# Optimization experiments

Hardware: AMD Instinct MI355X
Metric: run time of the kernel (lower is better)

The kernel has to match this reference:

```python
import jax, jax.numpy as jnp
import numpy as np

N_QUBITS = 20
EVO_SUPPORT = (2, 5)
CHAIN_QUBIT = 0


def _apply_operator(state, op, support):
    """Apply batched operator op (2^k, 2^k, B) to state (2,)*n + (B,) on `support` qubits.

    Faithful to pyqtorch's apply_operator: reshape op to (2,)*2k + (B,) and contract
    the support axes, keeping the batch axis aligned.
    """
    n = state.ndim - 1
    k = len(support)
    B = state.shape[-1]
    op = op.reshape((2,) * (2 * k) + (B,))
    letters = 'abcdefghijklmnopqrstuvwxyz'
    s_l = list(letters[:n])          # state qubit axes
    b = letters[n]                   # batch axis
    out_l = list(letters[n + 1:n + 1 + k])
    in_l = [s_l[q] for q in support]
    op_str = ''.join(out_l) + ''.join(in_l) + b
    st_str = ''.join(s_l) + b
    res = list(s_l)
    for q, o in zip(support, out_l):
        res[q] = o
    return jnp.einsum(f"{op_str},{st_str}->{''.join(res) + b}", op, state)


def setup_inputs() -> dict:
    key = jax.random.key(0)
    ks = jax.random.split(key, 6)
    B = 16
    dim = 2 ** N_QUBITS
    return {
        'state_re': jax.random.normal(ks[0], (dim, B), jnp.float32),
        'state_im': jax.random.normal(ks[1], (dim, B), jnp.float32),
        'hmat_re': jax.random.normal(ks[2], (4, 4, B), jnp.float32),
        'hmat_im': jax.random.normal(ks[3], (4, 4, B), jnp.float32),
        'theta': jax.random.uniform(ks[4], (8, B), jnp.float32),
        'tvals': jax.random.uniform(ks[5], (B,), jnp.float32),
    }


def reference(state_re, state_im, hmat_re, hmat_im, theta, tvals):
    n = N_QUBITS
    B = state_re.shape[-1]
    state = (state_re + 1j * state_im).astype(jnp.complex64).reshape((2,) * n + (B,))

    # --- PyQComposedBlock: chain of single-qubit RX gates composed via reduce(bmm, reversed) ---
    half = 0.5 * theta                      # (N_ops, B)
    c = jnp.cos(half).astype(jnp.complex64)
    s = jnp.sin(half).astype(jnp.complex64)
    # U_k: [[c, -i s], [-i s, c]] per op, batch-first layout (N_ops, B, 2, 2)
    U = jnp.stack([jnp.stack([c, -1j * s], axis=-1),
                   jnp.stack([-1j * s, c], axis=-1)], axis=-2)
    acc = U[-1]
    for i in range(U.shape[0] - 2, -1, -1):  # reduce(bmm, reversed(ops)): U_{N-1} @ ... @ U_0
        acc = acc @ U[i]
    state = _apply_operator(state, jnp.moveaxis(acc, 0, -1), (CHAIN_QUBIT,))

    # --- PyQHamiltonianEvolution: U = exp(-i t H) on a 2-qubit support ---
    A = (hmat_re + 1j * hmat_im).astype(jnp.complex64)       # (4, 4, B)
    H = 0.5 * (A + jnp.conj(jnp.swapaxes(A, 0, 1)))          # Hermitian generator
    Hb = jnp.moveaxis(H, -1, 0)                              # (B, 4, 4)
    evals, V = jnp.linalg.eigh(Hb)                           # H Hermitian -> exact matrix exp
    phase = jnp.exp(-1j * tvals[:, None] * evals)            # (B, 4)
    Ue = jnp.einsum('bij,bj,bkj->bik', V, phase.astype(jnp.complex64), jnp.conj(V))
    state = _apply_operator(state, jnp.moveaxis(Ue, 0, -1), EVO_SUPPORT)

    # --- Observable: total magnetization sum_q Z_q (AddPyQOperation of diagonal Z ops) ---
    w = jnp.zeros((2,) * n, jnp.float32)
    z = jnp.array([1.0, -1.0], jnp.float32)
    for q in range(n):
        w = w + z.reshape((1,) * q + (2,) + (1,) * (n - 1 - q))
    opsi = state * w[..., None]
    # expectation Re<psi|O|psi> per batch element
    return jnp.real(jnp.sum(jnp.conj(state) * opsi, axis=tuple(range(n))))
```

## Files before the change

### kernel.cpp

```cpp
#include <hip/hip_runtime.h>
#include <math.h>

constexpr int NQ     = 20;
constexpr int DIM    = 1 << NQ;
constexpr int B      = 16;
constexpr int GROUPS = 1 << 17;
constexpr int NBLK   = 1024;
constexpr int NTHR   = 512;


__global__ void prep_kernel(const float* __restrict__ hre, const float* __restrict__ him,
                            const float* __restrict__ theta, const float* __restrict__ tv,
                            float* __restrict__ ws) {
  int b = threadIdx.x;
  if (b >= B) return;

  double th = 0.0;
  for (int k = 0; k < 8; k++) th += (double)theta[k * B + b];
  th *= 0.5;
  ws[b]     = (float)cos(th);
  ws[B + b] = (float)sin(th);

  double t = (double)tv[b];
  double Mre[4][4], Mim[4][4];
  for (int i = 0; i < 4; i++)
    for (int j = 0; j < 4; j++) {
      double are = hre[(i*4+j)*B + b], aim = him[(i*4+j)*B + b];
      double cre = hre[(j*4+i)*B + b], cim = him[(j*4+i)*B + b];
      double Hre = 0.5*(are + cre), Him = 0.5*(aim - cim);
      Mre[i][j] = t * Him;
      Mim[i][j] = -t * Hre;
    }

  double ninf = 0.0;
  for (int i = 0; i < 4; i++) {
    double r = 0.0;
    for (int j = 0; j < 4; j++) r += fabs(Mre[i][j]) + fabs(Mim[i][j]);
    ninf = fmax(ninf, r);
  }
  int sc = 0;
  while (ninf > 0.25 && sc < 40) { ninf *= 0.5; sc++; }
  double scale = ldexp(1.0, -sc);
  for (int i = 0; i < 4; i++)
    for (int j = 0; j < 4; j++) { Mre[i][j] *= scale; Mim[i][j] *= scale; }

  double Tre[4][4], Tim[4][4];
  for (int i = 0; i < 4; i++)
    for (int j = 0; j < 4; j++) { Tre[i][j] = (i==j) ? 1.0 : 0.0; Tim[i][j] = 0.0; }
  for (int k = 13; k >= 1; k--) {
    double Pre[4][4], Pim[4][4];
    double inv = 1.0 / (double)k;
    for (int i = 0; i < 4; i++)
      for (int j = 0; j < 4; j++) {
        double rr = 0.0, ii = 0.0;
        for (int m = 0; m < 4; m++) {
          rr += Mre[i][m]*Tre[m][j] - Mim[i][m]*Tim[m][j];
          ii += Mre[i][m]*Tim[m][j] + Mim[i][m]*Tre[m][j];
        }
        Pre[i][j] = rr*inv + ((i==j) ? 1.0 : 0.0);
        Pim[i][j] = ii*inv;
      }
    for (int i = 0; i < 4; i++)
      for (int j = 0; j < 4; j++) { Tre[i][j] = Pre[i][j]; Tim[i][j] = Pim[i][j]; }
  }
  for (int q = 0; q < sc; q++) {
    double Pre[4][4], Pim[4][4];
    for (int i = 0; i < 4; i++)
      for (int j = 0; j < 4; j++) {
        double rr = 0.0, ii = 0.0;
        for (int m = 0; m < 4; m++) {
          rr += Tre[i][m]*Tre[m][j] - Tim[i][m]*Tim[m][j];
          ii += Tre[i][m]*Tim[m][j] + Tim[i][m]*Tre[m][j];
        }
        Pre[i][j] = rr; Pim[i][j] = ii;
      }
    for (int i = 0; i < 4; i++)
      for (int j = 0; j < 4; j++) { Tre[i][j] = Pre[i][j]; Tim[i][j] = Pim[i][j]; }
  }

  float* ue = ws + 2*B + b*32;
  for (int i = 0; i < 4; i++)
    for (int j = 0; j < 4; j++) {
      ue[(i*4+j)*2]     = (float)Tre[i][j];
      ue[(i*4+j)*2 + 1] = (float)Tim[i][j];
    }
}

#define RXPAIR(j, f) { \
  float xr = R[j].f, xi = I[j].f, yr = R[(j)+4].f, yi = I[(j)+4].f; \
  R[j].f     = fmaf(c4.f, xr,  s4.f * yi); \
  I[j].f     = fmaf(c4.f, xi, -s4.f * yr); \
  R[(j)+4].f = fmaf(s4.f, xi,  c4.f * yr); \
  I[(j)+4].f = fmaf(c4.f, yi, -s4.f * xr); \
}

#define UE_BI(f, bi, accv) \
  float accv = 0.f; \
  { \
    const float* ub = &u_lds[(b0 + (bi)) * 36]; \
    _Pragma("unroll") \
    for (int k = 0; k < 4; k++) { \
      float4 u0 = *(const float4*)(ub + 8*k);        \
      float4 u1 = *(const float4*)(ub + 8*k + 4);    \
      float rr0 = fmaf(u0.x, R[0].f, -u0.y * I[0].f); \
      rr0 = fmaf(u0.z, R[1].f, rr0); rr0 = fmaf(-u0.w, I[1].f, rr0); \
      rr0 = fmaf(u1.x, R[2].f, rr0); rr0 = fmaf(-u1.y, I[2].f, rr0); \
      rr0 = fmaf(u1.z, R[3].f, rr0); rr0 = fmaf(-u1.w, I[3].f, rr0); \
      float ii0 = fmaf(u0.x, I[0].f, u0.y * R[0].f); \
      ii0 = fmaf(u0.z, I[1].f, ii0); ii0 = fmaf(u0.w, R[1].f, ii0); \
      ii0 = fmaf(u1.x, I[2].f, ii0); ii0 = fmaf(u1.y, R[2].f, ii0); \
      ii0 = fmaf(u1.z, I[3].f, ii0); ii0 = fmaf(u1.w, R[3].f, ii0); \
      float rr1 = fmaf(u0.x, R[4].f, -u0.y * I[4].f); \
      rr1 = fmaf(u0.z, R[5].f, rr1); rr1 = fmaf(-u0.w, I[5].f, rr1); \
      rr1 = fmaf(u1.x, R[6].f, rr1); rr1 = fmaf(-u1.y, I[6].f, rr1); \
      rr1 = fmaf(u1.z, R[7].f, rr1); rr1 = fmaf(-u1.w, I[7].f, rr1); \
      float ii1 = fmaf(u0.x, I[4].f, u0.y * R[4].f); \
      ii1 = fmaf(u0.z, I[5].f, ii1); ii1 = fmaf(u0.w, R[5].f, ii1); \
      ii1 = fmaf(u1.x, I[6].f, ii1); ii1 = fmaf(u1.y, R[6].f, ii1); \
      ii1 = fmaf(u1.z, I[7].f, ii1); ii1 = fmaf(u1.w, R[7].f, ii1); \
      int sb = (k & 1) + (k >> 1); \
      float w0 = wb + (float)(3 - 2*sb);             \
      accv = fmaf(fmaf(rr0, rr0, ii0*ii0), w0,       accv); \
      accv = fmaf(fmaf(rr1, rr1, ii1*ii1), w0 - 2.f, accv); \
    } \
  }

__global__ __launch_bounds__(NTHR) void fused_kernel(
    const float* __restrict__ sre, const float* __restrict__ sim,
    const float* __restrict__ ws, float* __restrict__ partial) {
  __shared__ float u_lds[16 * 36];
  __shared__ float cs_lds[32];
  __shared__ float red[16];

  int t = threadIdx.x;
  {
    int b = t >> 5, e = t & 31;
    u_lds[b * 36 + e] = ws[2 * B + b * 32 + e];
  }
  if (t < 32) cs_lds[t] = ws[t];
  if (t < 16) red[t] = 0.f;
  __syncthreads();

  int tid = blockIdx.x * NTHR + t;
  int g   = tid >> 2;
  int b0  = (tid & 3) << 2;
  int base = (g & 0x3FFF) | ((g & 0xC000) << 1) | ((g & 0x10000) << 2);
  const float* pr = sre + base * B + b0;
  const float* pi = sim + base * B + b0;

  float4 R[8], I[8];
  #pragma unroll
  for (int j = 0; j < 8; j++) {
    int off = (((((j >> 2) & 1) << 19) | (((j >> 1) & 1) << 17) | ((j & 1) << 14))) * B;
    R[j] = *(const float4*)(pr + off);
    I[j] = *(const float4*)(pi + off);
  }

  float4 c4 = *(const float4*)&cs_lds[b0];
  float4 s4 = *(const float4*)&cs_lds[16 + b0];

  #pragma unroll
  for (int j = 0; j < 4; j++) {
    RXPAIR(j, x) RXPAIR(j, y) RXPAIR(j, z) RXPAIR(j, w)
  }

  int pc = __popc(base);
  float wb = (float)(17 - 2 * pc);

  UE_BI(x, 0, acc0)
  UE_BI(y, 1, acc1)
  UE_BI(z, 2, acc2)
  UE_BI(w, 3, acc3)

  #pragma unroll
  for (int m = 4; m <= 32; m <<= 1) {
    acc0 += __shfl_xor(acc0, m, 64);
    acc1 += __shfl_xor(acc1, m, 64);
    acc2 += __shfl_xor(acc2, m, 64);
    acc3 += __shfl_xor(acc3, m, 64);
  }

  if ((t & 63) < 4) {
    int bb = (t & 3) << 2;
    atomicAdd(&red[bb + 0], acc0);
    atomicAdd(&red[bb + 1], acc1);
    atomicAdd(&red[bb + 2], acc2);
    atomicAdd(&red[bb + 3], acc3);
  }
  __syncthreads();
  if (t < 16) partial[blockIdx.x * 16 + t] = red[t];
}

__global__ void reduce_kernel(const float* __restrict__ partial, float* __restrict__ out) {
  int t = threadIdx.x;
  int b = t & 15;
  float acc = 0.f;
  for (int i = t >> 4; i < NBLK; i += 16)
    acc += partial[i * 16 + b];
  acc += __shfl_xor(acc, 16, 64);
  acc += __shfl_xor(acc, 32, 64);
  __shared__ float red[16];
  if (t < 16) red[t] = 0.f;
  __syncthreads();
  if ((t & 63) < 16) atomicAdd(&red[t & 15], acc);
  __syncthreads();
  if (t < 16) out[t] = red[t];
}

extern "C" void kernel_launch(void* const* d_in, const int* in_sizes, int n_in,
                              void* d_out, int out_size, void* d_ws, size_t ws_size,
                              hipStream_t stream) {
  const float* sre = (const float*)d_in[0];
  const float* sim = (const float*)d_in[1];
  const float* hre = (const float*)d_in[2];
  const float* him = (const float*)d_in[3];
  const float* th  = (const float*)d_in[4];
  const float* tv  = (const float*)d_in[5];

  float* ws = (float*)d_ws;
  float* partial = ws + 544;

  prep_kernel<<<1, 64, 0, stream>>>(hre, him, th, tv, ws);
  fused_kernel<<<NBLK, NTHR, 0, stream>>>(sre, sim, ws, partial);
  reduce_kernel<<<1, 256, 0, stream>>>(partial, (float*)d_out);
}
```

Before: 191.1 us.

## Parallelize matrix-exp prep across threads and drop the separate reduce kernel

The 4x4 complex matrix exponential prep now runs with 256 threads, one per (batch, element), using shared-memory double buffers instead of a single serial thread per batch. The final reduction kernel is removed: each block atomically adds its partial sums straight into the output, which prep zeroes. The main kernel moves to 256-thread blocks with twice as many blocks and a min-occupancy hint. This removes one launch and the serial prep latency, at the cost of float atomics on 16 addresses from many blocks and a non-deterministic summation order.

Result: faster. 159.2 us (-16.7%).

```diff
diff --git a/kernel.cpp b/kernel.cpp
--- a/kernel.cpp
+++ b/kernel.cpp
@@ -5,85 +5,105 @@
 constexpr int DIM    = 1 << NQ;
 constexpr int B      = 16;
 constexpr int GROUPS = 1 << 17;
-constexpr int NBLK   = 1024;
-constexpr int NTHR   = 512;
-
-
-__global__ void prep_kernel(const float* __restrict__ hre, const float* __restrict__ him,
-                            const float* __restrict__ theta, const float* __restrict__ tv,
-                            float* __restrict__ ws) {
-  int b = threadIdx.x;
-  if (b >= B) return;
-
-  double th = 0.0;
-  for (int k = 0; k < 8; k++) th += (double)theta[k * B + b];
-  th *= 0.5;
-  ws[b]     = (float)cos(th);
-  ws[B + b] = (float)sin(th);
-
-  double t = (double)tv[b];
-  double Mre[4][4], Mim[4][4];
-  for (int i = 0; i < 4; i++)
-    for (int j = 0; j < 4; j++) {
-      double are = hre[(i*4+j)*B + b], aim = him[(i*4+j)*B + b];
-      double cre = hre[(j*4+i)*B + b], cim = him[(j*4+i)*B + b];
-      double Hre = 0.5*(are + cre), Him = 0.5*(aim - cim);
-      Mre[i][j] = t * Him;
-      Mim[i][j] = -t * Hre;
+constexpr int NBLK   = 2048;
+constexpr int NTHR   = 256;
+
+
+__global__ __launch_bounds__(256) void prep_kernel(
+    const float* __restrict__ hre, const float* __restrict__ him,
+    const float* __restrict__ theta, const float* __restrict__ tv,
+    float* __restrict__ ws, float* __restrict__ out) {
+  __shared__ double Mre[16][16], Mim[16][16];
+  __shared__ double Are[16][16], Aim[16][16];
+  __shared__ double Bre[16][16], Bim[16][16];
+  __shared__ double nrm[16][4];
+  __shared__ int    scl[16];
+  __shared__ int    scmax_s;
+
+  int t = threadIdx.x;
+  int b = t >> 4, e = t & 15, i = e >> 2, j = e & 3;
+
+  if (t < 16) out[t] = 0.f;
+  if (t == 0) scmax_s = 0;
+
+  if (e == 0) {
+    double th = 0.0;
+    for (int k = 0; k < 8; k++) th += (double)theta[k * B + b];
+    th *= 0.5;
+    ws[b]     = (float)cos(th);
+    ws[B + b] = (float)sin(th);
+  }
+
+  {
+    double tt  = (double)tv[b];
+    double are = hre[(i*4+j)*B + b], aim = him[(i*4+j)*B + b];
+    double cre = hre[(j*4+i)*B + b], cim = him[(j*4+i)*B + b];
+    double Hre = 0.5*(are + cre), Him = 0.5*(aim - cim);
+    Mre[b][e] = tt * Him;
+    Mim[b][e] = -tt * Hre;
+  }
+  __syncthreads();
+
+  if (j == 0) {
+    double r = 0.0;
+    for (int m = 0; m < 4; m++) r += fabs(Mre[b][i*4+m]) + fabs(Mim[b][i*4+m]);
+    nrm[b][i] = r;
+  }
+  __syncthreads();
+  if (e == 0) {
+    double ninf = fmax(fmax(nrm[b][0], nrm[b][1]), fmax(nrm[b][2], nrm[b][3]));
+    int sc = 0;
+    while (ninf > 0.25 && sc < 40) { ninf *= 0.5; sc++; }
+    scl[b] = sc;
+    atomicMax(&scmax_s, sc);
+  }
+  __syncthreads();
+  int sc = scl[b];
+  int scmax = scmax_s;
+  {
+    double scale = ldexp(1.0, -sc);
+    Mre[b][e] *= scale; Mim[b][e] *= scale;
+  }
+  Are[b][e] = (i == j) ? 1.0 : 0.0;
+  Aim[b][e] = 0.0;
+  __syncthreads();
+
+  double (*Tr)[16] = Are; double (*Ti)[16] = Aim;
+  double (*Pr)[16] = Bre; double (*Pi)[16] = Bim;
+
+  for (int k = 13; k >= 1; k--) {
+    double rr = 0.0, ii = 0.0;
+    for (int m = 0; m < 4; m++) {
+      double mr = Mre[b][i*4+m], mi = Mim[b][i*4+m];
+      double xr = Tr[b][m*4+j],  xi = Ti[b][m*4+j];
+      rr += mr*xr - mi*xi;
+      ii += mr*xi + mi*xr;
     }
-
-  double ninf = 0.0;
-  for (int i = 0; i < 4; i++) {
-    double r = 0.0;
-    for (int j = 0; j < 4; j++) r += fabs(Mre[i][j]) + fabs(Mim[i][j]);
-    ninf = fmax(ninf, r);
-  }
-  int sc = 0;
-  while (ninf > 0.25 && sc < 40) { ninf *= 0.5; sc++; }
-  double scale = ldexp(1.0, -sc);
-  for (int i = 0; i < 4; i++)
-    for (int j = 0; j < 4; j++) { Mre[i][j] *= scale; Mim[i][j] *= scale; }
-
-  double Tre[4][4], Tim[4][4];
-  for (int i = 0; i < 4; i++)
-    for (int j = 0; j < 4; j++) { Tre[i][j] = (i==j) ? 1.0 : 0.0; Tim[i][j] = 0.0; }
-  for (int k = 13; k >= 1; k--) {
-    double Pre[4][4], Pim[4][4];
     double inv = 1.0 / (double)k;
-    for (int i = 0; i < 4; i++)
-      for (int j = 0; j < 4; j++) {
-        double rr = 0.0, ii = 0.0;
-        for (int m = 0; m < 4; m++) {
-          rr += Mre[i][m]*Tre[m][j] - Mim[i][m]*Tim[m][j];
-          ii += Mre[i][m]*Tim[m][j] + Mim[i][m]*Tre[m][j];
-        }
-        Pre[i][j] = rr*inv + ((i==j) ? 1.0 : 0.0);
-        Pim[i][j] = ii*inv;
+    Pr[b][e] = rr*inv + ((i == j) ? 1.0 : 0.0);
+    Pi[b][e] = ii*inv;
+    { double (*s)[16] = Tr; Tr = Pr; Pr = s; s = Ti; Ti = Pi; Pi = s; }
+    __syncthreads();
+  }
+  for (int q = 0; q < scmax; q++) {
+    double rr, ii;
+    if (q < sc) {
+      rr = 0.0; ii = 0.0;
+      for (int m = 0; m < 4; m++) {
+        double xr = Tr[b][i*4+m], xi = Ti[b][i*4+m];
+        double yr = Tr[b][m*4+j], yi = Ti[b][m*4+j];
+        rr += xr*yr - xi*yi;
+        ii += xr*yi + xi*yr;
       }
-    for (int i = 0; i < 4; i++)
-      for (int j = 0; j < 4; j++) { Tre[i][j] = Pre[i][j]; Tim[i][j] = Pim[i][j]; }
-  }
-  for (int q = 0; q < sc; q++) {
-    double Pre[4][4], Pim[4][4];
-    for (int i = 0; i < 4; i++)
-      for (int j = 0; j < 4; j++) {
-        double rr = 0.0, ii = 0.0;
-        for (int m = 0; m < 4; m++) {
-          rr += Tre[i][m]*Tre[m][j] - Tim[i][m]*Tim[m][j];
-          ii += Tre[i][m]*Tim[m][j] + Tim[i][m]*Tre[m][j];
-        }
-        Pre[i][j] = rr; Pim[i][j] = ii;
-      }
-    for (int i = 0; i < 4; i++)
-      for (int j = 0; j < 4; j++) { Tre[i][j] = Pre[i][j]; Tim[i][j] = Pim[i][j]; }
+    } else { rr = Tr[b][e]; ii = Ti[b][e]; }
+    Pr[b][e] = rr; Pi[b][e] = ii;
+    { double (*s)[16] = Tr; Tr = Pr; Pr = s; s = Ti; Ti = Pi; Pi = s; }
+    __syncthreads();
   }
 
   float* ue = ws + 2*B + b*32;
-  for (int i = 0; i < 4; i++)
-    for (int j = 0; j < 4; j++) {
-      ue[(i*4+j)*2]     = (float)Tre[i][j];
-      ue[(i*4+j)*2 + 1] = (float)Tim[i][j];
-    }
+  ue[e*2]     = (float)Tr[b][e];
+  ue[e*2 + 1] = (float)Ti[b][e];
 }
 
 #define RXPAIR(j, f) { \
@@ -125,17 +145,18 @@
     } \
   }
 
-__global__ __launch_bounds__(NTHR) void fused_kernel(
+__global__ __launch_bounds__(NTHR, 3) void fused_kernel(
     const float* __restrict__ sre, const float* __restrict__ sim,
-    const float* __restrict__ ws, float* __restrict__ partial) {
+    const float* __restrict__ ws, float* __restrict__ out) {
   __shared__ float u_lds[16 * 36];
   __shared__ float cs_lds[32];
   __shared__ float red[16];
 
   int t = threadIdx.x;
   {
-    int b = t >> 5, e = t & 31;
-    u_lds[b * 36 + e] = ws[2 * B + b * 32 + e];
+    int bq = t & 15, e2 = t >> 4;
+    u_lds[bq * 36 + e2 * 2]     = ws[2 * B + bq * 32 + e2 * 2];
+    u_lds[bq * 36 + e2 * 2 + 1] = ws[2 * B + bq * 32 + e2 * 2 + 1];
   }
   if (t < 32) cs_lds[t] = ws[t];
   if (t < 16) red[t] = 0.f;
@@ -188,23 +209,7 @@
     atomicAdd(&red[bb + 3], acc3);
   }
   __syncthreads();
-  if (t < 16) partial[blockIdx.x * 16 + t] = red[t];
-}
-
-__global__ void reduce_kernel(const float* __restrict__ partial, float* __restrict__ out) {
-  int t = threadIdx.x;
-  int b = t & 15;
-  float acc = 0.f;
-  for (int i = t >> 4; i < NBLK; i += 16)
-    acc += partial[i * 16 + b];
-  acc += __shfl_xor(acc, 16, 64);
-  acc += __shfl_xor(acc, 32, 64);
-  __shared__ float red[16];
-  if (t < 16) red[t] = 0.f;
-  __syncthreads();
-  if ((t & 63) < 16) atomicAdd(&red[t & 15], acc);
-  __syncthreads();
-  if (t < 16) out[t] = red[t];
+  if (t < 16) atomicAdd(&out[t], red[t]);
 }
 
 extern "C" void kernel_launch(void* const* d_in, const int* in_sizes, int n_in,
@@ -218,9 +223,8 @@
   const float* tv  = (const float*)d_in[5];
 
   float* ws = (float*)d_ws;
-  float* partial = ws + 544;
-
-  prep_kernel<<<1, 64, 0, stream>>>(hre, him, th, tv, ws);
-  fused_kernel<<<NBLK, NTHR, 0, stream>>>(sre, sim, ws, partial);
-  reduce_kernel<<<1, 256, 0, stream>>>(partial, (float*)d_out);
-}
+  float* out = (float*)d_out;
+
+  prep_kernel<<<1, 256, 0, stream>>>(hre, him, th, tv, ws, out);
+  fused_kernel<<<NBLK, NTHR, 0, stream>>>(sre, sim, ws, out);
+}
```
